# Kernel tuning notes

Measured on AMD Instinct MI355X. Metric: run time of the kernel, lower is better.

Reference implementation:

```python
import jax, jax.numpy as jnp
import numpy as np

NG, NQ, E, H, L, B = 500000, 100000, 1000000, 128, 4, 1024
EMB, GDIM, NTYPES = 16, 32, 31


def _xavier(key, shape):
    fan_in, fan_out = shape[-2], shape[-1]
    lim = float(np.sqrt(6.0 / (fan_in + fan_out)))
    return jax.random.uniform(key, shape, minval=-lim, maxval=lim, dtype=jnp.float32)


def setup_inputs():
    key = jax.random.key(0)
    ks = iter(jax.random.split(key, 64))
    nk = lambda: next(ks)
    inp = {}
    inp["gate_type_idx"] = jax.random.randint(nk(), (NG,), 0, NTYPES)
    inp["gate_arity"] = jax.random.randint(nk(), (NG,), 1, 3)
    inp["gate_is_directional"] = jax.random.randint(nk(), (NG,), 0, 2)
    inp["gate_index_norm"] = jax.random.uniform(nk(), (NG,), dtype=jnp.float32)
    inp["qubit_degree_norm"] = jax.random.uniform(nk(), (NQ,), dtype=jnp.float32)
    inp["src_g2q"] = jax.random.randint(nk(), (E,), 0, NG)
    inp["dst_g2q"] = jax.random.randint(nk(), (E,), 0, NQ)
    inp["src_q2g"] = jax.random.randint(nk(), (E,), 0, NQ)
    inp["dst_q2g"] = jax.random.randint(nk(), (E,), 0, NG)
    inp["gate_batch"] = jnp.sort(jax.random.randint(nk(), (NG,), 0, B))
    inp["qubit_batch"] = jnp.sort(jax.random.randint(nk(), (NQ,), 0, B))
    inp["global_features"] = jax.random.normal(nk(), (B, GDIM), dtype=jnp.float32)
    inp["backend_bit"] = jax.random.randint(nk(), (B,), 0, 2).astype(jnp.float32)
    inp["precision_bit"] = jax.random.randint(nk(), (B,), 0, 2).astype(jnp.float32)
    inp["emb_table"] = jax.random.normal(nk(), (NTYPES, EMB), dtype=jnp.float32) / np.sqrt(EMB).astype(np.float32)
    inp["gate_proj_W"] = _xavier(nk(), (EMB + 3, H)); inp["gate_proj_b"] = jnp.zeros((H,), jnp.float32)
    inp["qubit_proj_W"] = _xavier(nk(), (1, H)); inp["qubit_proj_b"] = jnp.zeros((H,), jnp.float32)
    inp["g2q_ll_W"] = _xavier(nk(), (L, H, H)); inp["g2q_ll_b"] = jnp.zeros((L, H), jnp.float32)
    inp["g2q_lr_W"] = _xavier(nk(), (L, H, H)); inp["g2q_lr_b"] = jnp.zeros((L, H), jnp.float32)
    inp["q2g_ll_W"] = _xavier(nk(), (L, H, H)); inp["q2g_ll_b"] = jnp.zeros((L, H), jnp.float32)
    inp["q2g_lr_W"] = _xavier(nk(), (L, H, H)); inp["q2g_lr_b"] = jnp.zeros((L, H), jnp.float32)
    inp["gate_ln_g"] = jnp.ones((L, H), jnp.float32); inp["gate_ln_b"] = jnp.zeros((L, H), jnp.float32)
    inp["qubit_ln_g"] = jnp.ones((L, H), jnp.float32); inp["qubit_ln_b"] = jnp.zeros((L, H), jnp.float32)
    inp["glob_W"] = _xavier(nk(), (GDIM, H)); inp["glob_b"] = jnp.zeros((H,), jnp.float32)
    inp["backbone_W"] = _xavier(nk(), (5 * H + 2, H)); inp["backbone_b"] = jnp.zeros((H,), jnp.float32)
    inp["thr_W"] = _xavier(nk(), (H, 10)); inp["thr_b"] = jnp.zeros((10,), jnp.float32)
    inp["run_W"] = _xavier(nk(), (H, 1)); inp["run_b"] = jnp.zeros((1,), jnp.float32)
    return inp


def _layernorm(x, g, b, eps=1e-5):
    m = x.mean(-1, keepdims=True)
    v = jnp.mean((x - m) ** 2, axis=-1, keepdims=True)
    return (x - m) * jax.lax.rsqrt(v + eps) * g + b


def _seg_mean(x, idx, n):
    s = jax.ops.segment_sum(x, idx, num_segments=n)
    c = jax.ops.segment_sum(jnp.ones((x.shape[0], 1), x.dtype), idx, num_segments=n)
    return s / jnp.maximum(c, 1.0)


def reference(gate_type_idx, gate_arity, gate_is_directional, gate_index_norm,
              qubit_degree_norm, src_g2q, dst_g2q, src_q2g, dst_q2g,
              gate_batch, qubit_batch, global_features, backend_bit, precision_bit,
              emb_table, gate_proj_W, gate_proj_b, qubit_proj_W, qubit_proj_b,
              g2q_ll_W, g2q_ll_b, g2q_lr_W, g2q_lr_b,
              q2g_ll_W, q2g_ll_b, q2g_lr_W, q2g_lr_b,
              gate_ln_g, gate_ln_b, qubit_ln_g, qubit_ln_b,
              glob_W, glob_b, backbone_W, backbone_b, thr_W, thr_b, run_W, run_b):
    gate_feat = jnp.concatenate([
        emb_table[gate_type_idx],
        gate_arity[:, None].astype(jnp.float32),
        gate_is_directional[:, None].astype(jnp.float32),
        gate_index_norm[:, None]], axis=1)                      # [NG, EMB+3]
    gx = gate_feat @ gate_proj_W + gate_proj_b                  # [NG, H]
    qx = qubit_degree_norm[:, None] @ qubit_proj_W + qubit_proj_b  # [NQ, H]
    for l in range(L):
        # SAGEConv((H,H),H) per edge type: mean-aggregate src msgs, lin_l(agg)+lin_r(x_dst)
        agg_q = _seg_mean(gx[src_g2q], dst_g2q, NQ)
        q_new = agg_q @ g2q_ll_W[l] + g2q_ll_b[l] + qx @ g2q_lr_W[l] + g2q_lr_b[l]
        agg_g = _seg_mean(qx[src_q2g], dst_q2g, NG)
        g_new = agg_g @ q2g_ll_W[l] + q2g_ll_b[l] + gx @ q2g_lr_W[l] + q2g_lr_b[l]
        gx = _layernorm(jax.nn.silu(g_new), gate_ln_g[l], gate_ln_b[l]) + gx
        qx = _layernorm(jax.nn.silu(q_new), qubit_ln_g[l], qubit_ln_b[l]) + qx
    gm = _seg_mean(gx, gate_batch, B)
    gstd = jnp.sqrt(jnp.maximum(_seg_mean(gx * gx, gate_batch, B) - gm * gm, 1e-6))
    qm = _seg_mean(qx, qubit_batch, B)
    qstd = jnp.sqrt(jnp.maximum(_seg_mean(qx * qx, qubit_batch, B) - qm * qm, 1e-6))
    glob = jax.nn.silu(global_features @ glob_W + glob_b)
    combined = jnp.concatenate([gm, gstd, qm, qstd, glob,
                                backend_bit[:, None], precision_bit[:, None]], axis=1)
    feat = jax.nn.silu(combined @ backbone_W + backbone_b)
    threshold_logits = feat @ thr_W + thr_b                     # [B, 10]
    log_runtime = (feat @ run_W + run_b)[:, 0]                  # [B]
    return threshold_logits, log_runtime
```

## Files before the change

### kernel.cpp

```cpp
#include <hip/hip_runtime.h>
#include <hip/hip_bf16.h>


#define NGATE 500000
#define NQUB  100000
#define NEDGE 1000000
#define H     128
#define NL    4
#define NB    1024
#define EMB   16
#define GDIM  32
#define NTYPES 31

typedef unsigned int u32;
typedef unsigned short u16;
typedef __attribute__((ext_vector_type(8))) short short8;
typedef __attribute__((ext_vector_type(4))) float f32x4;

__device__ __forceinline__ float silu_f(float x) { return x / (1.f + __expf(-x)); }
__device__ __forceinline__ u16 f2bf(float f) {
  __hip_bfloat16 h = __float2bfloat16(f);
  u16 r;
  __builtin_memcpy(&r, &h, 2);
  return r;
}
__device__ __forceinline__ u32 pack2(float a, float b) {
  return (u32)f2bf(a) | ((u32)f2bf(b) << 16);
}
__device__ __forceinline__ float2 unpack2(u32 v) {
  return make_float2(__uint_as_float((v & 0xffffu) << 16), __uint_as_float((v >> 16) << 16));
}
__device__ __forceinline__ float bf16tof(u16 h) { return __uint_as_float(((u32)h) << 16); }

__global__ void k_sentinel(float* out) { out[0] = 10000.f; }


__global__ __launch_bounds__(256) void k_gate_proj(
    const int* __restrict__ ty, const int* __restrict__ ar, const int* __restrict__ di,
    const float* __restrict__ ixn, const float* __restrict__ emb,
    const float* __restrict__ W, const float* __restrict__ bias, u32* __restrict__ gx) {
  __shared__ float sW[19 * H];
  __shared__ float se[NTYPES * EMB];
  __shared__ float sb[H];
  for (int i = threadIdx.x; i < 19 * H; i += 256) sW[i] = W[i];
  for (int i = threadIdx.x; i < NTYPES * EMB; i += 256) se[i] = emb[i];
  if (threadIdx.x < H) sb[threadIdx.x] = bias[threadIdx.x];
  __syncthreads();
  const float2* sW2 = (const float2*)sW;
  const float2* sb2 = (const float2*)sb;
  int lane = threadIdx.x & 63, wid = threadIdx.x >> 6;
  int gw = blockIdx.x * 4 + wid, nw = gridDim.x * 4;
  for (int r = gw; r < NGATE; r += nw) {
    int t = ty[r];
    float fa = (float)ar[r], fd = (float)di[r], fi = ixn[r];
    float2 b2v = sb2[lane];
    float al = b2v.x, ah = b2v.y;
#pragma unroll
    for (int k = 0; k < EMB; k++) {
      float e = se[t * EMB + k];
      float2 w = sW2[k * 64 + lane];
      al += e * w.x;
      ah += e * w.y;
    }
    float2 wa = sW2[16 * 64 + lane], wd = sW2[17 * 64 + lane], wi = sW2[18 * 64 + lane];
    al += fa * wa.x + fd * wd.x + fi * wi.x;
    ah += fa * wa.y + fd * wd.y + fi * wi.y;
    gx[(size_t)r * 64 + lane] = pack2(al, ah);
  }
}

__global__ __launch_bounds__(256) void k_qubit_proj(
    const float* __restrict__ deg, const float* __restrict__ W,
    const float* __restrict__ b, u32* __restrict__ qx) {
  int idx = blockIdx.x * 256 + threadIdx.x;
  if (idx >= NQUB * 64) return;
  int r = idx >> 6, l = idx & 63;
  float d = deg[r];
  qx[idx] = pack2(d * W[2 * l] + b[2 * l], d * W[2 * l + 1] + b[2 * l + 1]);
}


__global__ __launch_bounds__(256) void k_count(
    const int* __restrict__ dq, const int* __restrict__ dg,
    int* __restrict__ cq, int* __restrict__ cg) {
  int e = blockIdx.x * 256 + threadIdx.x;
  if (e >= NEDGE) return;
  atomicAdd(&cq[dq[e]], 1);
  atomicAdd(&cg[dg[e]], 1);
}

__global__ __launch_bounds__(1024) void k_scan_chunk(
    const int* __restrict__ cnt, int n, int* __restrict__ out, int* __restrict__ bsum) {
  __shared__ int s[1024];
  int i = blockIdx.x * 1024 + threadIdx.x;
  int v = (i < n) ? cnt[i] : 0;
  s[threadIdx.x] = v;
  __syncthreads();
  for (int d = 1; d < 1024; d <<= 1) {
    int t = (threadIdx.x >= d) ? s[threadIdx.x - d] : 0;
    __syncthreads();
    s[threadIdx.x] += t;
    __syncthreads();
  }
  if (i < n) out[i] = s[threadIdx.x];
  if (threadIdx.x == 1023 && bsum) bsum[blockIdx.x] = s[1023];
}

__global__ __launch_bounds__(1024) void k_scan_add(
    int n, int* __restrict__ off, const int* __restrict__ bscan) {
  int i = blockIdx.x * 1024 + threadIdx.x;
  if (i < n && blockIdx.x > 0) off[i + 1] += bscan[blockIdx.x - 1];
  if (i == 0) off[0] = 0;
}

__global__ __launch_bounds__(256) void k_csr_fill(
    const int* __restrict__ sq, const int* __restrict__ dq,
    const int* __restrict__ sg, const int* __restrict__ dg,
    const int* __restrict__ offq, const int* __restrict__ offg,
    int* __restrict__ fq, int* __restrict__ fg,
    int* __restrict__ csrq, int* __restrict__ csrg) {
  int e = blockIdx.x * 256 + threadIdx.x;
  if (e >= NEDGE) return;
  int d1 = dq[e];
  int p1 = atomicAdd(&fq[d1], 1);
  csrq[offq[d1] + p1] = sq[e];
  int d2 = dg[e];
  int p2 = atomicAdd(&fg[d2], 1);
  csrg[offg[d2] + p2] = sg[e];
}


__global__ __launch_bounds__(256) void k_prep_w(
    const float* __restrict__ g2q_ll, const float* __restrict__ g2q_lr,
    const float* __restrict__ q2g_ll, const float* __restrict__ q2g_lr,
    u16* __restrict__ Whi, u16* __restrict__ Wlo) {
  int t = blockIdx.x * 256 + threadIdx.x;
  if (t >= 8 * 256 * 128) return;
  int o = t & 127, k = (t >> 7) & 255, mat = t >> 15;
  int l = mat >> 1, side = mat & 1;
  const float* Wll = side ? q2g_ll : g2q_ll;
  const float* Wlr = side ? q2g_lr : g2q_lr;
  float w = (k < 128) ? Wll[((size_t)l * 128 + k) * 128 + o]
                      : Wlr[((size_t)l * 128 + (k - 128)) * 128 + o];
  u16 hi = f2bf(w);
  float lof = w - bf16tof(hi);
  int ks = k >> 5, kr = k & 31, ot = o >> 4;
  int lane = ((kr >> 3) << 4) | (o & 15);
  int j = kr & 7;
  size_t pos = (((size_t)(mat * 8 + ks) * 8 + ot) * 64 + lane) * 8 + j;
  Whi[pos] = hi;
  Wlo[pos] = f2bf(lof);
}

__global__ __launch_bounds__(256) void k_prep_b(
    const float* __restrict__ g2q_llb, const float* __restrict__ g2q_lrb,
    const float* __restrict__ q2g_llb, const float* __restrict__ q2g_lrb,
    float* __restrict__ bcat) {
  int t = blockIdx.x * 256 + threadIdx.x;
  if (t >= 8 * 128) return;
  int c = t & 127, mat = t >> 7, l = mat >> 1, side = mat & 1;
  bcat[t] = side ? (q2g_llb[l * 128 + c] + q2g_lrb[l * 128 + c])
                 : (g2q_llb[l * 128 + c] + g2q_lrb[l * 128 + c]);
}


__global__ __launch_bounds__(256) void k_gather_rows(
    const u32* __restrict__ SRC, const int* __restrict__ off, const int* __restrict__ csr,
    u32* __restrict__ OUT, int n) {
  int lane = threadIdx.x & 63, wid = threadIdx.x >> 6;
  int w = blockIdx.x * 4 + wid, nw = gridDim.x * 4;
  for (int r = w; r < n; r += nw) {
    int b = off[r], e = off[r + 1];
    float sl = 0.f, sh = 0.f;
    for (int t = b; t < e; t += 4) {
      int t1 = min(t + 1, e - 1), t2 = min(t + 2, e - 1), t3 = min(t + 3, e - 1);
      float w1 = (t + 1 < e) ? 1.f : 0.f;
      float w2 = (t + 2 < e) ? 1.f : 0.f;
      float w3 = (t + 3 < e) ? 1.f : 0.f;
      u32 v0 = SRC[(size_t)csr[t] * 64 + lane];
      u32 v1 = SRC[(size_t)csr[t1] * 64 + lane];
      u32 v2 = SRC[(size_t)csr[t2] * 64 + lane];
      u32 v3 = SRC[(size_t)csr[t3] * 64 + lane];
      float2 f0 = unpack2(v0), f1 = unpack2(v1), f2 = unpack2(v2), f3 = unpack2(v3);
      sl += f0.x + w1 * f1.x + w2 * f2.x + w3 * f3.x;
      sh += f0.y + w1 * f1.y + w2 * f2.y + w3 * f3.y;
    }
    float inv = 1.f / fmaxf((float)(e - b), 1.f);
    OUT[(size_t)r * 64 + lane] = pack2(sl * inv, sh * inv);
  }
}


template <int GATHER>
__global__ __launch_bounds__(256, 2) void k_layer(
    const u16* __restrict__ AGG16, const u16* __restrict__ SRC16,
    const int* __restrict__ off, const int* __restrict__ csr,
    u32* __restrict__ X, const u16* __restrict__ Whi, const u16* __restrict__ Wlo,
    const float* __restrict__ bcat, const float* __restrict__ lng,
    const float* __restrict__ lnb, int nrows) {
  __shared__ __align__(16) u16 sB[2][2][4096];
  int tid = threadIdx.x;
  int lane = tid & 63, wid = tid >> 6;
  long wt = (long)blockIdx.x * 4 + wid;
  long r0 = wt * 32;
  bool wvalid = (r0 < nrows);
  long r0c = wvalid ? r0 : 0;
  int rlo = lane & 15, khi = lane >> 4;
  u16* X16 = (u16*)X;

  uint4 h0, h1, l0, l1;
#define LOADB(KS) { \
    const uint4* sh_ = (const uint4*)(Whi + (size_t)(KS) * 4096); \
    const uint4* sl_ = (const uint4*)(Wlo + (size_t)(KS) * 4096); \
    h0 = sh_[tid]; h1 = sh_[256 + tid]; l0 = sl_[tid]; l1 = sl_[256 + tid]; }
#define WRITEB(BUF) { \
    ((uint4*)sB[BUF][0])[tid] = h0; ((uint4*)sB[BUF][0])[256 + tid] = h1; \
    ((uint4*)sB[BUF][1])[tid] = l0; ((uint4*)sB[BUF][1])[256 + tid] = l1; }

  LOADB(0);
  WRITEB(0);
  LOADB(1);

  short8 ag[2][4], xg[2][4];
#pragma unroll
  for (int rs = 0; rs < 2; rs++) {
    long row = r0c + rs * 16 + rlo;
#pragma unroll
    for (int ks = 0; ks < 4; ks++)
      xg[rs][ks] = *(const short8*)(X16 + row * 128 + ks * 32 + khi * 8);
    if (GATHER == 0) {
#pragma unroll
      for (int ks = 0; ks < 4; ks++)
        ag[rs][ks] = *(const short8*)(AGG16 + row * 128 + ks * 32 + khi * 8);
    } else {
      int bgn = off[row], end = off[row + 1];
      float m[4][8];
#pragma unroll
      for (int ks = 0; ks < 4; ks++)
#pragma unroll
        for (int j = 0; j < 8; j++) m[ks][j] = 0.f;
      for (int t = bgn; t < end; t += 2) {
        int t1 = min(t + 1, end - 1);
        float w1 = (t + 1 < end) ? 1.f : 0.f;
        const u16* p0 = SRC16 + (size_t)csr[t] * 128 + khi * 8;
        const u16* p1 = SRC16 + (size_t)csr[t1] * 128 + khi * 8;
        uint4 va[4] = {*(const uint4*)(p0), *(const uint4*)(p0 + 32),
                       *(const uint4*)(p0 + 64), *(const uint4*)(p0 + 96)};
        uint4 vb[4] = {*(const uint4*)(p1), *(const uint4*)(p1 + 32),
                       *(const uint4*)(p1 + 64), *(const uint4*)(p1 + 96)};
#pragma unroll
        for (int ks = 0; ks < 4; ks++) {
          m[ks][0] += __uint_as_float((va[ks].x & 0xffffu) << 16) + w1 * __uint_as_float((vb[ks].x & 0xffffu) << 16);
          m[ks][1] += __uint_as_float((va[ks].x >> 16) << 16) + w1 * __uint_as_float((vb[ks].x >> 16) << 16);
          m[ks][2] += __uint_as_float((va[ks].y & 0xffffu) << 16) + w1 * __uint_as_float((vb[ks].y & 0xffffu) << 16);
          m[ks][3] += __uint_as_float((va[ks].y >> 16) << 16) + w1 * __uint_as_float((vb[ks].y >> 16) << 16);
          m[ks][4] += __uint_as_float((va[ks].z & 0xffffu) << 16) + w1 * __uint_as_float((vb[ks].z & 0xffffu) << 16);
          m[ks][5] += __uint_as_float((va[ks].z >> 16) << 16) + w1 * __uint_as_float((vb[ks].z >> 16) << 16);
          m[ks][6] += __uint_as_float((va[ks].w & 0xffffu) << 16) + w1 * __uint_as_float((vb[ks].w & 0xffffu) << 16);
          m[ks][7] += __uint_as_float((va[ks].w >> 16) << 16) + w1 * __uint_as_float((vb[ks].w >> 16) << 16);
        }
      }
      float inv = 1.f / fmaxf((float)(end - bgn), 1.f);
#pragma unroll
      for (int ks = 0; ks < 4; ks++) {
        short8 af;
#pragma unroll
        for (int j = 0; j < 8; j++) af[j] = (short)f2bf(m[ks][j] * inv);
        ag[rs][ks] = af;
      }
    }
  }

  __syncthreads();

  f32x4 acc[2][8];
#pragma unroll
  for (int rs = 0; rs < 2; rs++)
#pragma unroll
    for (int ot = 0; ot < 8; ot++) acc[rs][ot] = (f32x4){0.f, 0.f, 0.f, 0.f};

#pragma unroll
  for (int ks = 0; ks < 8; ks++) {
    const u16* sH = sB[ks & 1][0];
    const u16* sL = sB[ks & 1][1];
    short8 a0 = (ks < 4) ? ag[0][ks & 3] : xg[0][ks & 3];
    short8 a1 = (ks < 4) ? ag[1][ks & 3] : xg[1][ks & 3];
#pragma unroll
    for (int ot = 0; ot < 8; ot++) {
      short8 bh = *(const short8*)(sH + ot * 512 + lane * 8);
      short8 bl = *(const short8*)(sL + ot * 512 + lane * 8);
      acc[0][ot] = __builtin_amdgcn_mfma_f32_16x16x32_bf16(a0, bh, acc[0][ot], 0, 0, 0);
      acc[0][ot] = __builtin_amdgcn_mfma_f32_16x16x32_bf16(a0, bl, acc[0][ot], 0, 0, 0);
      acc[1][ot] = __builtin_amdgcn_mfma_f32_16x16x32_bf16(a1, bh, acc[1][ot], 0, 0, 0);
      acc[1][ot] = __builtin_amdgcn_mfma_f32_16x16x32_bf16(a1, bl, acc[1][ot], 0, 0, 0);
    }
    if (ks < 7) {
      WRITEB((ks + 1) & 1);
      if (ks < 6) LOADB(ks + 2);
      __syncthreads();
    }
  }
#undef LOADB
#undef WRITEB

  if (!wvalid) return;
  float bz[8], lg[8], lb[8];
#pragma unroll
  for (int ot = 0; ot < 8; ot++) {
    int c = ot * 16 + rlo;
    bz[ot] = bcat[c];
    lg[ot] = lng[c];
    lb[ot] = lnb[c];
  }
#pragma unroll
  for (int rs = 0; rs < 2; rs++) {
#pragma unroll
    for (int i = 0; i < 4; i++) {
      long row = r0 + rs * 16 + khi * 4 + i;
      float u[8], s1 = 0.f, s2 = 0.f;
#pragma unroll
      for (int ot = 0; ot < 8; ot++) {
        float z = acc[rs][ot][i] + bz[ot];
        float uu = silu_f(z);
        u[ot] = uu;
        s1 += uu;
        s2 += uu * uu;
      }
#pragma unroll
      for (int msk = 1; msk < 16; msk <<= 1) {
        s1 += __shfl_xor(s1, msk, 64);
        s2 += __shfl_xor(s2, msk, 64);
      }
      float mean = s1 * (1.f / 128.f);
      float var = s2 * (1.f / 128.f) - mean * mean;
      float rsq = rsqrtf(var + 1e-5f);
#pragma unroll
      for (int ot = 0; ot < 8; ot++) {
        size_t idx = (size_t)row * 128 + ot * 16 + rlo;
        float xr = bf16tof(X16[idx]);
        float o = (u[ot] - mean) * rsq * lg[ot] + lb[ot] + xr;
        X16[idx] = f2bf(o);
      }
    }
  }
}


__global__ __launch_bounds__(256) void k_seg_counts(
    const int* __restrict__ batch, float* __restrict__ bcnt, int n) {
  int t = blockIdx.x * 256 + threadIdx.x;
  int r0 = t * 64;
  if (r0 >= n) return;
  int end = min(r0 + 64, n);
  int cur = batch[r0];
  float c = 0.f;
  for (int r = r0; r < end; r++) {
    int b = batch[r];
    if (b != cur) { atomicAdd(&bcnt[cur], c); cur = b; c = 0.f; }
    c += 1.f;
  }
  atomicAdd(&bcnt[cur], c);
}

__global__ __launch_bounds__(128) void k_bstats(
    const u32* __restrict__ X, const int* __restrict__ batch,
    float* __restrict__ bsum, float* __restrict__ bsq, int nrows) {
  __shared__ int sb[32];
  int r0 = blockIdx.x * 32;
  int c = threadIdx.x;
  if (c < 32) sb[c] = (r0 + c < nrows) ? batch[r0 + c] : -1;
  __syncthreads();
  float s = 0.f, q = 0.f;
  int cur = sb[0];
  const u16* Xh = (const u16*)X;
  for (int i = 0; i < 32; i++) {
    int r = r0 + i;
    if (r >= nrows) break;
    int b = sb[i];
    if (b != cur) {
      atomicAdd(&bsum[cur * H + c], s);
      atomicAdd(&bsq[cur * H + c], q);
      s = 0.f; q = 0.f; cur = b;
    }
    float v = bf16tof(Xh[(size_t)r * H + c]);
    s += v;
    q += v * v;
  }
  atomicAdd(&bsum[cur * H + c], s);
  atomicAdd(&bsq[cur * H + c], q);
}

__global__ __launch_bounds__(128) void k_head(
    const float* __restrict__ bsum_g, const float* __restrict__ bsq_g, const float* __restrict__ bcnt_g,
    const float* __restrict__ bsum_q, const float* __restrict__ bsq_q, const float* __restrict__ bcnt_q,
    const float* __restrict__ gf, const float* __restrict__ backend, const float* __restrict__ precision,
    const float* __restrict__ globW, const float* __restrict__ globb,
    const float* __restrict__ bbW, const float* __restrict__ bbb,
    const float* __restrict__ thrW, const float* __restrict__ thrb,
    const float* __restrict__ runW, const float* __restrict__ runb,
    float* __restrict__ out) {
  __shared__ float comb[5 * H + 2];
  __shared__ float feat[H];
  int b = blockIdx.x, c = threadIdx.x;
  float ig = 1.f / fmaxf(bcnt_g[b], 1.f);
  float iq = 1.f / fmaxf(bcnt_q[b], 1.f);
  float gm = bsum_g[b * H + c] * ig;
  float gs = sqrtf(fmaxf(bsq_g[b * H + c] * ig - gm * gm, 1e-6f));
  float qm = bsum_q[b * H + c] * iq;
  float qs = sqrtf(fmaxf(bsq_q[b * H + c] * iq - qm * qm, 1e-6f));
  float gl = globb[c];
#pragma unroll
  for (int j = 0; j < GDIM; j++) gl += gf[b * GDIM + j] * globW[j * H + c];
  gl = silu_f(gl);
  comb[c] = gm;
  comb[H + c] = gs;
  comb[2 * H + c] = qm;
  comb[3 * H + c] = qs;
  comb[4 * H + c] = gl;
  if (c == 0) {
    comb[5 * H] = backend[b];
    comb[5 * H + 1] = precision[b];
  }
  __syncthreads();
  float f = bbb[c];
  for (int k = 0; k < 5 * H + 2; k++) f += comb[k] * bbW[k * H + c];
  f = silu_f(f);
  feat[c] = f;
  __syncthreads();
  if (c < 10) {
    float o = thrb[c];
#pragma unroll
    for (int k = 0; k < H; k++) o += feat[k] * thrW[k * 10 + c];
    out[b * 10 + c] = o;
  }
  if (c == 64) {
    float o = runb[0];
    for (int k = 0; k < H; k++) o += feat[k] * runW[k];
    out[NB * 10 + b] = o;
  }
}


extern "C" void kernel_launch(void* const* d_in, const int* in_sizes, int n_in,
                              void* d_out, int out_size, void* d_ws, size_t ws_size,
                              hipStream_t stream) {
  const int* gate_type = (const int*)d_in[0];
  const int* gate_arity = (const int*)d_in[1];
  const int* gate_dir = (const int*)d_in[2];
  const float* gate_ixn = (const float*)d_in[3];
  const float* qdeg = (const float*)d_in[4];
  const int* src_g2q = (const int*)d_in[5];
  const int* dst_g2q = (const int*)d_in[6];
  const int* src_q2g = (const int*)d_in[7];
  const int* dst_q2g = (const int*)d_in[8];
  const int* gate_batch = (const int*)d_in[9];
  const int* qubit_batch = (const int*)d_in[10];
  const float* gfeat = (const float*)d_in[11];
  const float* backend = (const float*)d_in[12];
  const float* precision = (const float*)d_in[13];
  const float* emb = (const float*)d_in[14];
  const float* gpW = (const float*)d_in[15];
  const float* gpb = (const float*)d_in[16];
  const float* qpW = (const float*)d_in[17];
  const float* qpb = (const float*)d_in[18];
  const float* g2q_ll_W = (const float*)d_in[19];
  const float* g2q_ll_b = (const float*)d_in[20];
  const float* g2q_lr_W = (const float*)d_in[21];
  const float* g2q_lr_b = (const float*)d_in[22];
  const float* q2g_ll_W = (const float*)d_in[23];
  const float* q2g_ll_b = (const float*)d_in[24];
  const float* q2g_lr_W = (const float*)d_in[25];
  const float* q2g_lr_b = (const float*)d_in[26];
  const float* gate_ln_g = (const float*)d_in[27];
  const float* gate_ln_b = (const float*)d_in[28];
  const float* qubit_ln_g = (const float*)d_in[29];
  const float* qubit_ln_b = (const float*)d_in[30];
  const float* globW = (const float*)d_in[31];
  const float* globb = (const float*)d_in[32];
  const float* bbW = (const float*)d_in[33];
  const float* bbb = (const float*)d_in[34];
  const float* thrW = (const float*)d_in[35];
  const float* thrb = (const float*)d_in[36];
  const float* runW = (const float*)d_in[37];
  const float* runb = (const float*)d_in[38];

  char* base = (char*)d_ws;
  u32* gx    = (u32*)base;
  u32* qx    = gx + (size_t)NGATE * 64;
  u32* agg_q = qx + (size_t)NQUB * 64;
  u16* Whi   = (u16*)(agg_q + (size_t)NQUB * 64);
  u16* Wlo   = Whi + 8 * 32768;
  float* bcat = (float*)(Wlo + 8 * 32768);
  int* offq = (int*)(bcat + 8 * 128);
  int* offg = offq + (NQUB + 1);
  int* csrq = offg + (NGATE + 1);
  int* csrg = csrq + NEDGE;
  int* cntq = csrg + NEDGE;
  int* cntg = cntq + NQUB;
  int* bsumA = cntg + NGATE;
  int* bsumB = bsumA + 512;
  float* bsum_g = (float*)(bsumB + 512);
  float* bsq_g  = bsum_g + NB * H;
  float* bsum_q = bsq_g + NB * H;
  float* bsq_q  = bsum_q + NB * H;
  float* bcnt_g = bsq_q + NB * H;
  float* bcnt_q = bcnt_g + NB;
  size_t need = (size_t)((char*)(bcnt_q + NB) - base);
  if (ws_size < need) {
    k_sentinel<<<1, 1, 0, stream>>>((float*)d_out);
    return;
  }

  k_prep_w<<<(8 * 256 * 128 + 255) / 256, 256, 0, stream>>>(
      g2q_ll_W, g2q_lr_W, q2g_ll_W, q2g_lr_W, Whi, Wlo);
  k_prep_b<<<4, 256, 0, stream>>>(g2q_ll_b, g2q_lr_b, q2g_ll_b, q2g_lr_b, bcat);

  hipMemsetAsync(cntq, 0, (size_t)(NQUB + NGATE) * sizeof(int), stream);
  k_count<<<(NEDGE + 255) / 256, 256, 0, stream>>>(dst_g2q, dst_q2g, cntq, cntg);
  const int nbq = (NQUB + 1023) / 1024, nbg = (NGATE + 1023) / 1024;
  k_scan_chunk<<<nbq, 1024, 0, stream>>>(cntq, NQUB, offq + 1, bsumA);
  k_scan_chunk<<<1, 1024, 0, stream>>>(bsumA, nbq, bsumB, nullptr);
  k_scan_add<<<nbq, 1024, 0, stream>>>(NQUB, offq, bsumB);
  k_scan_chunk<<<nbg, 1024, 0, stream>>>(cntg, NGATE, offg + 1, bsumA);
  k_scan_chunk<<<1, 1024, 0, stream>>>(bsumA, nbg, bsumB, nullptr);
  k_scan_add<<<nbg, 1024, 0, stream>>>(NGATE, offg, bsumB);
  hipMemsetAsync(cntq, 0, (size_t)(NQUB + NGATE) * sizeof(int), stream);
  k_csr_fill<<<(NEDGE + 255) / 256, 256, 0, stream>>>(
      src_g2q, dst_g2q, src_q2g, dst_q2g, offq, offg, cntq, cntg, csrq, csrg);

  size_t stats_floats = 4ULL * NB * H + 2ULL * NB;
  hipMemsetAsync(bsum_g, 0, stats_floats * sizeof(float), stream);
  k_seg_counts<<<(NGATE / 64 + 256) / 256, 256, 0, stream>>>(gate_batch, bcnt_g, NGATE);
  k_seg_counts<<<(NQUB / 64 + 256) / 256, 256, 0, stream>>>(qubit_batch, bcnt_q, NQUB);

  k_gate_proj<<<1024, 256, 0, stream>>>(gate_type, gate_arity, gate_dir, gate_ixn,
                                        emb, gpW, gpb, gx);
  k_qubit_proj<<<(NQUB * 64 + 255) / 256, 256, 0, stream>>>(qdeg, qpW, qpb, qx);

  const int blocks_g = (NGATE + 127) / 128;
  const int blocks_q = (NQUB + 127) / 128;
  for (int l = 0; l < NL; l++) {
    const u16* WhiG = Whi + (size_t)(l * 2 + 1) * 32768;
    const u16* WloG = Wlo + (size_t)(l * 2 + 1) * 32768;
    const float* bcG = bcat + (l * 2 + 1) * 128;
    const u16* WhiQ = Whi + (size_t)(l * 2) * 32768;
    const u16* WloQ = Wlo + (size_t)(l * 2) * 32768;
    const float* bcQ = bcat + (l * 2) * 128;
    k_gather_rows<<<(NQUB + 3) / 4, 256, 0, stream>>>(gx, offq, csrq, agg_q, NQUB);
    k_layer<1><<<blocks_g, 256, 0, stream>>>(
        nullptr, (const u16*)qx, offg, csrg, gx,
        WhiG, WloG, bcG, gate_ln_g + (size_t)l * H, gate_ln_b + (size_t)l * H, NGATE);
    k_layer<0><<<blocks_q, 256, 0, stream>>>(
        (const u16*)agg_q, nullptr, nullptr, nullptr, qx,
        WhiQ, WloQ, bcQ, qubit_ln_g + (size_t)l * H, qubit_ln_b + (size_t)l * H, NQUB);
  }

  k_bstats<<<NGATE / 32, 128, 0, stream>>>(gx, gate_batch, bsum_g, bsq_g, NGATE);
  k_bstats<<<NQUB / 32, 128, 0, stream>>>(qx, qubit_batch, bsum_q, bsq_q, NQUB);
  k_head<<<NB, 128, 0, stream>>>(bsum_g, bsq_g, bcnt_g, bsum_q, bsq_q, bcnt_q,
                                 gfeat, backend, precision, globW, globb,
                                 bbW, bbb, thrW, thrb, runW, runb, (float*)d_out);
}
```

Before: 1.347 ms.

## Fuse qubit gather into layer kernel and snapshot qx for gate update

Removes the separate k_gather_rows kernel and the agg_q intermediate by always performing the CSR mean-gather inside k_layer. The qubit layer now runs first, gathering from the old gx, and a device copy of qx is taken beforehand so the gate layer still aggregates the pre-update qubit features. Launch bounds rise to 4 blocks per SIMD to raise occupancy. The cost is an extra 25.6MB device-to-device copy per layer and possible register spilling under the tighter bound.

```diff
diff --git a/kernel.cpp b/kernel.cpp
--- a/kernel.cpp
+++ b/kernel.cpp
@@ -164,36 +164,8 @@
 }
 
 
-__global__ __launch_bounds__(256) void k_gather_rows(
-    const u32* __restrict__ SRC, const int* __restrict__ off, const int* __restrict__ csr,
-    u32* __restrict__ OUT, int n) {
-  int lane = threadIdx.x & 63, wid = threadIdx.x >> 6;
-  int w = blockIdx.x * 4 + wid, nw = gridDim.x * 4;
-  for (int r = w; r < n; r += nw) {
-    int b = off[r], e = off[r + 1];
-    float sl = 0.f, sh = 0.f;
-    for (int t = b; t < e; t += 4) {
-      int t1 = min(t + 1, e - 1), t2 = min(t + 2, e - 1), t3 = min(t + 3, e - 1);
-      float w1 = (t + 1 < e) ? 1.f : 0.f;
-      float w2 = (t + 2 < e) ? 1.f : 0.f;
-      float w3 = (t + 3 < e) ? 1.f : 0.f;
-      u32 v0 = SRC[(size_t)csr[t] * 64 + lane];
-      u32 v1 = SRC[(size_t)csr[t1] * 64 + lane];
-      u32 v2 = SRC[(size_t)csr[t2] * 64 + lane];
-      u32 v3 = SRC[(size_t)csr[t3] * 64 + lane];
-      float2 f0 = unpack2(v0), f1 = unpack2(v1), f2 = unpack2(v2), f3 = unpack2(v3);
-      sl += f0.x + w1 * f1.x + w2 * f2.x + w3 * f3.x;
-      sh += f0.y + w1 * f1.y + w2 * f2.y + w3 * f3.y;
-    }
-    float inv = 1.f / fmaxf((float)(e - b), 1.f);
-    OUT[(size_t)r * 64 + lane] = pack2(sl * inv, sh * inv);
-  }
-}
-
-
-template <int GATHER>
-__global__ __launch_bounds__(256, 2) void k_layer(
-    const u16* __restrict__ AGG16, const u16* __restrict__ SRC16,
+__global__ __launch_bounds__(256, 4) void k_layer(
+    const u16* __restrict__ SRC16,
     const int* __restrict__ off, const int* __restrict__ csr,
     u32* __restrict__ X, const u16* __restrict__ Whi, const u16* __restrict__ Wlo,
     const float* __restrict__ bcat, const float* __restrict__ lng,
@@ -228,46 +200,40 @@
 #pragma unroll
     for (int ks = 0; ks < 4; ks++)
       xg[rs][ks] = *(const short8*)(X16 + row * 128 + ks * 32 + khi * 8);
-    if (GATHER == 0) {
-#pragma unroll
-      for (int ks = 0; ks < 4; ks++)
-        ag[rs][ks] = *(const short8*)(AGG16 + row * 128 + ks * 32 + khi * 8);
-    } else {
-      int bgn = off[row], end = off[row + 1];
-      float m[4][8];
-#pragma unroll
-      for (int ks = 0; ks < 4; ks++)
-#pragma unroll
-        for (int j = 0; j < 8; j++) m[ks][j] = 0.f;
-      for (int t = bgn; t < end; t += 2) {
-        int t1 = min(t + 1, end - 1);
-        float w1 = (t + 1 < end) ? 1.f : 0.f;
-        const u16* p0 = SRC16 + (size_t)csr[t] * 128 + khi * 8;
-        const u16* p1 = SRC16 + (size_t)csr[t1] * 128 + khi * 8;
-        uint4 va[4] = {*(const uint4*)(p0), *(const uint4*)(p0 + 32),
-                       *(const uint4*)(p0 + 64), *(const uint4*)(p0 + 96)};
-        uint4 vb[4] = {*(const uint4*)(p1), *(const uint4*)(p1 + 32),
-                       *(const uint4*)(p1 + 64), *(const uint4*)(p1 + 96)};
-#pragma unroll
-        for (int ks = 0; ks < 4; ks++) {
-          m[ks][0] += __uint_as_float((va[ks].x & 0xffffu) << 16) + w1 * __uint_as_float((vb[ks].x & 0xffffu) << 16);
-          m[ks][1] += __uint_as_float((va[ks].x >> 16) << 16) + w1 * __uint_as_float((vb[ks].x >> 16) << 16);
-          m[ks][2] += __uint_as_float((va[ks].y & 0xffffu) << 16) + w1 * __uint_as_float((vb[ks].y & 0xffffu) << 16);
-          m[ks][3] += __uint_as_float((va[ks].y >> 16) << 16) + w1 * __uint_as_float((vb[ks].y >> 16) << 16);
-          m[ks][4] += __uint_as_float((va[ks].z & 0xffffu) << 16) + w1 * __uint_as_float((vb[ks].z & 0xffffu) << 16);
-          m[ks][5] += __uint_as_float((va[ks].z >> 16) << 16) + w1 * __uint_as_float((vb[ks].z >> 16) << 16);
-          m[ks][6] += __uint_as_float((va[ks].w & 0xffffu) << 16) + w1 * __uint_as_float((vb[ks].w & 0xffffu) << 16);
-          m[ks][7] += __uint_as_float((va[ks].w >> 16) << 16) + w1 * __uint_as_float((vb[ks].w >> 16) << 16);
-        }
+    int bgn = off[row], end = off[row + 1];
+    float m[4][8];
+#pragma unroll
+    for (int ks = 0; ks < 4; ks++)
+#pragma unroll
+      for (int j = 0; j < 8; j++) m[ks][j] = 0.f;
+    for (int t = bgn; t < end; t += 2) {
+      int t1 = min(t + 1, end - 1);
+      float w1 = (t + 1 < end) ? 1.f : 0.f;
+      const u16* p0 = SRC16 + (size_t)csr[t] * 128 + khi * 8;
+      const u16* p1 = SRC16 + (size_t)csr[t1] * 128 + khi * 8;
+      uint4 va[4] = {*(const uint4*)(p0), *(const uint4*)(p0 + 32),
+                     *(const uint4*)(p0 + 64), *(const uint4*)(p0 + 96)};
+      uint4 vb[4] = {*(const uint4*)(p1), *(const uint4*)(p1 + 32),
+                     *(const uint4*)(p1 + 64), *(const uint4*)(p1 + 96)};
+#pragma unroll
+      for (int ks = 0; ks < 4; ks++) {
+        m[ks][0] += __uint_as_float((va[ks].x & 0xffffu) << 16) + w1 * __uint_as_float((vb[ks].x & 0xffffu) << 16);
+        m[ks][1] += __uint_as_float((va[ks].x >> 16) << 16) + w1 * __uint_as_float((vb[ks].x >> 16) << 16);
+        m[ks][2] += __uint_as_float((va[ks].y & 0xffffu) << 16) + w1 * __uint_as_float((vb[ks].y & 0xffffu) << 16);
+        m[ks][3] += __uint_as_float((va[ks].y >> 16) << 16) + w1 * __uint_as_float((vb[ks].y >> 16) << 16);
+        m[ks][4] += __uint_as_float((va[ks].z & 0xffffu) << 16) + w1 * __uint_as_float((vb[ks].z & 0xffffu) << 16);
+        m[ks][5] += __uint_as_float((va[ks].z >> 16) << 16) + w1 * __uint_as_float((vb[ks].z >> 16) << 16);
+        m[ks][6] += __uint_as_float((va[ks].w & 0xffffu) << 16) + w1 * __uint_as_float((vb[ks].w & 0xffffu) << 16);
+        m[ks][7] += __uint_as_float((va[ks].w >> 16) << 16) + w1 * __uint_as_float((vb[ks].w >> 16) << 16);
       }
-      float inv = 1.f / fmaxf((float)(end - bgn), 1.f);
-#pragma unroll
-      for (int ks = 0; ks < 4; ks++) {
-        short8 af;
-#pragma unroll
-        for (int j = 0; j < 8; j++) af[j] = (short)f2bf(m[ks][j] * inv);
-        ag[rs][ks] = af;
-      }
+    }
+    float inv = 1.f / fmaxf((float)(end - bgn), 1.f);
+#pragma unroll
+    for (int ks = 0; ks < 4; ks++) {
+      short8 af;
+#pragma unroll
+      for (int j = 0; j < 8; j++) af[j] = (short)f2bf(m[ks][j] * inv);
+      ag[rs][ks] = af;
     }
   }
 
@@ -487,8 +453,8 @@
   char* base = (char*)d_ws;
   u32* gx    = (u32*)base;
   u32* qx    = gx + (size_t)NGATE * 64;
-  u32* agg_q = qx + (size_t)NQUB * 64;
-  u16* Whi   = (u16*)(agg_q + (size_t)NQUB * 64);
+  u32* qx_old= qx + (size_t)NQUB * 64;
+  u16* Whi   = (u16*)(qx_old + (size_t)NQUB * 64);
   u16* Wlo   = Whi + 8 * 32768;
   float* bcat = (float*)(Wlo + 8 * 32768);
   int* offq = (int*)(bcat + 8 * 128);
@@ -546,13 +512,14 @@
     const u16* WhiQ = Whi + (size_t)(l * 2) * 32768;
     const u16* WloQ = Wlo + (size_t)(l * 2) * 32768;
     const float* bcQ = bcat + (l * 2) * 128;
-    k_gather_rows<<<(NQUB + 3) / 4, 256, 0, stream>>>(gx, offq, csrq, agg_q, NQUB);
-    k_layer<1><<<blocks_g, 256, 0, stream>>>(
-        nullptr, (const u16*)qx, offg, csrg, gx,
+    hipMemcpyAsync(qx_old, qx, (size_t)NQUB * 64 * sizeof(u32),
+                   hipMemcpyDeviceToDevice, stream);
+    k_layer<<<blocks_q, 256, 0, stream>>>(
+        (const u16*)gx, offq, csrq, qx,
+        WhiQ, WloQ, bcQ, qubit_ln_g + (size_t)l * H, qubit_ln_b + (size_t)l * H, NQUB);
+    k_layer<<<blocks_g, 256, 0, stream>>>(
+        (const u16*)qx_old, offg, csrg, gx,
         WhiG, WloG, bcG, gate_ln_g + (size_t)l * H, gate_ln_b + (size_t)l * H, NGATE);
-    k_layer<0><<<blocks_q, 256, 0, stream>>>(
-        (const u16*)agg_q, nullptr, nullptr, nullptr, qx,
-        WhiQ, WloQ, bcQ, qubit_ln_g + (size_t)l * H, qubit_ln_b + (size_t)l * H, NQUB);
   }
 
   k_bstats<<<NGATE / 32, 128, 0, stream>>>(gx, gate_batch, bsum_g, bsq_g, NGATE);
```

New measurement: 1.592 ms. 1.18x slower.
